# Performance work log

Measured on AMD Instinct MI355X. Metric: run time of the kernel, lower is better.

The kernel has to match this reference:

```python
import jax, jax.numpy as jnp
import numpy as np

B, N, C, H = 4, 1024, 768, 12
D = C // H
SCALE = D ** -0.5


def setup_inputs() -> dict:
    key = jax.random.key(0)
    k1, k2, k3, k4 = jax.random.split(key, 4)
    x1 = jax.random.normal(k1, (B, N, C), dtype=jnp.float32)
    x2 = jax.random.normal(k2, (B, N, C), dtype=jnp.float32)
    # shared (dual-stream) Linear2 weights, torch nn.Linear layout: [out, in]
    W_qkv = jax.random.normal(k3, (3 * C, C), dtype=jnp.float32) * (C ** -0.5)
    b_qkv = jnp.zeros((3 * C,), dtype=jnp.float32)
    W_proj = jax.random.normal(k4, (C, C), dtype=jnp.float32) * (C ** -0.5)
    b_proj = jnp.zeros((C,), dtype=jnp.float32)
    return {"x1": x1, "x2": x2, "W_qkv": W_qkv, "b_qkv": b_qkv,
            "W_proj": W_proj, "b_proj": b_proj}


def _split_qkv(x, W_qkv, b_qkv):
    qkv = (x @ W_qkv.T + b_qkv).reshape(B, N, 3, H, D)
    qkv = jnp.transpose(qkv, (2, 0, 3, 1, 4))  # [3,B,H,N,D]
    return qkv[0], qkv[1], qkv[2]


def reference(x1, x2, W_qkv, b_qkv, W_proj, b_proj):
    q1, k1, v1 = _split_qkv(x1, W_qkv, b_qkv)
    q2, k2, v2 = _split_qkv(x2, W_qkv, b_qkv)
    # two score maps, combined before a single shared softmax
    s1 = jnp.einsum("bhqd,bhkd->bhqk", q1 * SCALE, k1)
    s2 = jnp.einsum("bhqd,bhkd->bhqk", q2 * SCALE, k2)
    attn = jax.nn.softmax(s1 + s2, axis=-1)  # [B,H,N,N]
    # same attention matrix applied to both value streams
    o1 = jnp.einsum("bhqk,bhkd->bhqd", attn, v1)
    o2 = jnpum = jnp.einsum("bhqk,bhkd->bhqd", attn, v2) if False else jnp.einsum("bhqk,bhkd->bhqd", attn, v2)
    o1 = jnp.transpose(o1, (0, 2, 1, 3)).reshape(B, N, C)
    o2 = jnp.transpose(o2, (0, 2, 1, 3)).reshape(B, N, C)
    y1 = o1 @ W_proj.T + b_proj
    y2 = o2 @ W_proj.T + b_proj
    return y1, y2
```

## Files before the change

### kernel.cpp

```cpp
#include <hip/hip_runtime.h>
#include <hip/hip_bf16.h>


typedef __bf16 bf16x8 __attribute__((ext_vector_type(8)));
typedef __bf16 bf16x4 __attribute__((ext_vector_type(4)));
typedef float  f32x4  __attribute__((ext_vector_type(4)));

__device__ __forceinline__ bf16x8 cvt8(const float* p) {
    f32x4 f0 = *(const f32x4*)p;
    f32x4 f1 = *(const f32x4*)(p + 4);
    bf16x8 r;
    r[0] = (__bf16)f0[0]; r[1] = (__bf16)f0[1]; r[2] = (__bf16)f0[2]; r[3] = (__bf16)f0[3];
    r[4] = (__bf16)f1[0]; r[5] = (__bf16)f1[1]; r[6] = (__bf16)f1[2]; r[7] = (__bf16)f1[3];
    return r;
}

__device__ __forceinline__ void async16(const __bf16* g, __bf16* l) {
    __builtin_amdgcn_global_load_lds(
        (const __attribute__((address_space(1))) void*)g,
        (__attribute__((address_space(3))) void*)l, 16, 0, 0);
}

__global__ __launch_bounds__(256)
void cvt3_k(const float* __restrict__ x1, const float* __restrict__ x2,
            const float* __restrict__ wq, __bf16* __restrict__ xc,
            __bf16* __restrict__ wqc)
{
    int bid = blockIdx.x;
    const float* src; __bf16* dst; int i;
    if (bid < 1536)      { src = x1; dst = xc;             i = (bid * 256 + threadIdx.x) * 8; }
    else if (bid < 3072) { src = x2; dst = xc + 3145728;   i = ((bid - 1536) * 256 + threadIdx.x) * 8; }
    else                 { src = wq; dst = wqc;            i = ((bid - 3072) * 256 + threadIdx.x) * 8; }
    *(bf16x8*)(dst + i) = cvt8(src + i);
}

__global__ __launch_bounds__(256)
void cvt_k(const float* __restrict__ src, __bf16* __restrict__ dst, int n) {
    int i = (blockIdx.x * 256 + threadIdx.x) * 8;
    if (i < n) *(bf16x8*)(dst + i) = cvt8(src + i);
}

__global__ __launch_bounds__(256)
void gemm_qkv_s(const __bf16* __restrict__ Xc, const __bf16* __restrict__ Wq,
                const float* __restrict__ bias,
                __bf16* __restrict__ qo, __bf16* __restrict__ ko,
                __bf16* __restrict__ vo)
{
    constexpr int K = 768;
    __shared__ __bf16 As[128 * 32];
    __shared__ __bf16 Bs[128 * 32];

    const int t = threadIdx.x, w = t >> 6, lane = t & 63;
    const int l15 = lane & 15, quad = lane >> 4;
    const int wm = w >> 1, wn = w & 1;

    const int bid  = blockIdx.x;
    const int xcd  = bid & 7;
    const int i6   = bid >> 3;
    const int pair = i6 / 18;
    const int gx   = i6 - pair * 18;
    const int p    = xcd * 8 + pair;
    const int gy   = p & 31;
    const int st   = p >> 5;

    const int lrow = lane >> 2, lcol = (lane & 3) * 8;

    const __bf16* Ab = Xc + (size_t)st * 3145728 + (size_t)(gy * 128) * K;
    const __bf16* Bb = Wq + (size_t)(gx * 128) * K;

    f32x4 acc[4][4];
#pragma unroll
    for (int mi = 0; mi < 4; mi++)
#pragma unroll
        for (int ni = 0; ni < 4; ni++) acc[mi][ni] = f32x4{0.f, 0.f, 0.f, 0.f};

    for (int k0 = 0; k0 < K; k0 += 32) {
#pragma unroll
        for (int i = 0; i < 2; i++) {
            int r = w * 32 + i * 16 + lrow;
            async16(Ab + (size_t)r * K + k0 + lcol, &As[r * 32 + lcol]);
            async16(Bb + (size_t)r * K + k0 + lcol, &Bs[r * 32 + lcol]);
        }
        __syncthreads();
        bf16x8 af[4], bfr[4];
#pragma unroll
        for (int mi = 0; mi < 4; mi++)
            af[mi] = *(const bf16x8*)&As[(wm * 64 + mi * 16 + l15) * 32 + quad * 8];
#pragma unroll
        for (int ni = 0; ni < 4; ni++)
            bfr[ni] = *(const bf16x8*)&Bs[(wn * 64 + ni * 16 + l15) * 32 + quad * 8];
#pragma unroll
        for (int mi = 0; mi < 4; mi++)
#pragma unroll
            for (int ni = 0; ni < 4; ni++)
                acc[mi][ni] = __builtin_amdgcn_mfma_f32_16x16x32_bf16(af[mi], bfr[ni], acc[mi][ni], 0, 0, 0);
        __syncthreads();
    }

    const int which = (gx * 128) / 768;

    if (which == 2) {
#pragma unroll
        for (int ni = 0; ni < 4; ni++) {
            int j = gx * 128 + wn * 64 + ni * 16 + l15;
            int c = j - 1536;
            int h = c >> 6, d = c & 63;
            float bj = bias[j];
#pragma unroll
            for (int mi = 0; mi < 4; mi++) {
                int row0 = gy * 128 + wm * 64 + mi * 16 + quad * 4;
                int b = row0 >> 10, tok0 = row0 & 1023;
                bf16x4 pv;
#pragma unroll
                for (int r = 0; r < 4; r++) pv[r] = (__bf16)(acc[mi][ni][r] + bj);
                *(bf16x4*)&vo[((size_t)((st * 4 + b) * 12 + h) * 64 + d) * 1024 + tok0] = pv;
            }
        }
    } else {
#pragma unroll
        for (int ni = 0; ni < 4; ni++) {
            int j     = gx * 128 + wn * 64 + ni * 16 + l15;
            int c     = j - which * 768;
            int h = c >> 6, d = c & 63;
            float bj  = bias[j];
#pragma unroll
            for (int mi = 0; mi < 4; mi++) {
#pragma unroll
                for (int r = 0; r < 4; r++) {
                    int row = gy * 128 + wm * 64 + mi * 16 + quad * 4 + r;
                    int b = row >> 10, tok = row & 1023;
                    float val = acc[mi][ni][r] + bj;
                    if (which == 0)
                        qo[((size_t)((st * 4 + b) * 12 + h) * 1024 + tok) * 64 + d] = (__bf16)(val * 0.125f);
                    else
                        ko[((size_t)((st * 4 + b) * 12 + h) * 1024 + tok) * 64 + d] = (__bf16)val;
                }
            }
        }
    }
}

__global__ __launch_bounds__(256)
void gemm_proj(const __bf16* __restrict__ A, const __bf16* __restrict__ Wp,
               const float* __restrict__ bias, float* __restrict__ out)
{
    constexpr int K = 768;
    __shared__ __bf16 As[128 * 32];
    __shared__ __bf16 Bs[128 * 32];

    const int t = threadIdx.x, w = t >> 6, lane = t & 63;
    const int l15 = lane & 15, quad = lane >> 4;
    const int wm = w >> 1, wn = w & 1;
    const int gx = blockIdx.x, gy = blockIdx.y;
    const int lrow = lane >> 2, lcol = (lane & 3) * 8;

    const __bf16* Ab = A  + (size_t)(gy * 128) * K;
    const __bf16* Bb = Wp + (size_t)(gx * 128) * K;

    f32x4 acc[4][4];
#pragma unroll
    for (int mi = 0; mi < 4; mi++)
#pragma unroll
        for (int ni = 0; ni < 4; ni++) acc[mi][ni] = f32x4{0.f, 0.f, 0.f, 0.f};

    for (int k0 = 0; k0 < K; k0 += 32) {
#pragma unroll
        for (int i = 0; i < 2; i++) {
            int r = w * 32 + i * 16 + lrow;
            async16(Ab + (size_t)r * K + k0 + lcol, &As[r * 32 + lcol]);
            async16(Bb + (size_t)r * K + k0 + lcol, &Bs[r * 32 + lcol]);
        }
        __syncthreads();
        bf16x8 af[4], bfr[4];
#pragma unroll
        for (int mi = 0; mi < 4; mi++)
            af[mi] = *(const bf16x8*)&As[(wm * 64 + mi * 16 + l15) * 32 + quad * 8];
#pragma unroll
        for (int ni = 0; ni < 4; ni++)
            bfr[ni] = *(const bf16x8*)&Bs[(wn * 64 + ni * 16 + l15) * 32 + quad * 8];
#pragma unroll
        for (int mi = 0; mi < 4; mi++)
#pragma unroll
            for (int ni = 0; ni < 4; ni++)
                acc[mi][ni] = __builtin_amdgcn_mfma_f32_16x16x32_bf16(af[mi], bfr[ni], acc[mi][ni], 0, 0, 0);
        __syncthreads();
    }

#pragma unroll
    for (int ni = 0; ni < 4; ni++) {
        int col  = gx * 128 + wn * 64 + ni * 16 + l15;
        float bj = bias[col];
#pragma unroll
        for (int mi = 0; mi < 4; mi++)
#pragma unroll
            for (int r = 0; r < 4; r++) {
                int row = gy * 128 + wm * 64 + mi * 16 + quad * 4 + r;
                out[(size_t)row * 768 + col] = acc[mi][ni][r] + bj;
            }
    }
}

__global__ __launch_bounds__(128, 2)
void attn_k(const __bf16* __restrict__ qws, const __bf16* __restrict__ kws,
            const __bf16* __restrict__ vws, __bf16* __restrict__ ows)
{
    __shared__ __bf16 Ks[2][2][2][2][512];
    __shared__ __bf16 Vs[2][2][4][512];
    __shared__ __bf16 Ps[2][2][16 * 72];

    const int g  = blockIdx.x;
    const int qt = g / 48;
    const int bh = g % 48;
    const int b = bh / 12, h = bh % 12;
    const int t = threadIdx.x, w = t >> 6, lane = t & 63;
    const int l15 = lane & 15, quad = lane >> 4;

    const size_t head_off = (size_t)bh * 65536;
    const size_t ss       = (size_t)48 * 65536;

    bf16x8 qf[2][2][2];
#pragma unroll
    for (int set = 0; set < 2; set++)
#pragma unroll
        for (int s = 0; s < 2; s++)
#pragma unroll
            for (int kk = 0; kk < 2; kk++)
                qf[set][s][kk] = *(const bf16x8*)(qws + s * ss + head_off
                    + (size_t)(qt * 64 + w * 32 + set * 16 + l15) * 64 + kk * 32 + quad * 8);

    float lsum[2] = {0.f, 0.f};
    f32x4 accO[2][2][4];
#pragma unroll
    for (int set = 0; set < 2; set++)
#pragma unroll
        for (int s = 0; s < 2; s++)
#pragma unroll
            for (int mi = 0; mi < 4; mi++) accO[set][s][mi] = f32x4{0.f, 0.f, 0.f, 0.f};

    const __bf16* kbase = kws + head_off;
    const __bf16* vbase = vws + head_off;

#define STAGE_TILE(BUF, KEYB)                                                   \
    do {                                                                        \
        if (w == 0) {                                                           \
            _Pragma("unroll")                                                   \
            for (int i = 0; i < 8; i++) {                                       \
                const int s = i >> 2, kk = (i >> 1) & 1, mi = i & 1;            \
                async16(kbase + s * ss + (size_t)((KEYB) + mi * 16 + l15) * 64  \
                            + kk * 32 + quad * 8,                               \
                        &Ks[BUF][s][kk][mi][lane * 8]);                         \
            }                                                                   \
        } else {                                                                \
            _Pragma("unroll")                                                   \
            for (int i = 0; i < 8; i++) {                                       \
                const int s = i >> 2, mi = i & 3;                               \
                async16(vbase + s * ss + (size_t)(mi * 16 + l15) * 1024         \
                            + (KEYB) + quad * 8,                                \
                        &Vs[BUF][s][mi][lane * 8]);                             \
            }                                                                   \
        }                                                                       \
    } while (0)

    STAGE_TILE(0, 0);
    __syncthreads();

#pragma unroll 2
    for (int kt = 0; kt < 32; kt++) {
        const int cb = kt & 1, nb = cb ^ 1;

        if (kt < 31) STAGE_TILE(nb, (kt + 1) * 32);

        f32x4 accS[2][2];
#pragma unroll
        for (int set = 0; set < 2; set++)
#pragma unroll
            for (int mi = 0; mi < 2; mi++) accS[set][mi] = f32x4{0.f, 0.f, 0.f, 0.f};
        __builtin_amdgcn_s_setprio(1);
#pragma unroll
        for (int s = 0; s < 2; s++)
#pragma unroll
            for (int kk = 0; kk < 2; kk++) {
                bf16x8 kf0 = *(const bf16x8*)&Ks[cb][s][kk][0][lane * 8];
                bf16x8 kf1 = *(const bf16x8*)&Ks[cb][s][kk][1][lane * 8];
#pragma unroll
                for (int set = 0; set < 2; set++) {
                    accS[set][0] = __builtin_amdgcn_mfma_f32_16x16x32_bf16(kf0, qf[set][s][kk], accS[set][0], 0, 0, 0);
                    accS[set][1] = __builtin_amdgcn_mfma_f32_16x16x32_bf16(kf1, qf[set][s][kk], accS[set][1], 0, 0, 0);
                }
            }
        __builtin_amdgcn_s_setprio(0);

#pragma unroll
        for (int set = 0; set < 2; set++) {
            float rs = 0.f;
#pragma unroll
            for (int mi = 0; mi < 2; mi++) {
                bf16x4 pk;
#pragma unroll
                for (int r = 0; r < 4; r++) {
                    float pv = __expf(accS[set][mi][r]);
                    pk[r] = (__bf16)pv;
                    rs += pv;
                }
                *(bf16x4*)&Ps[w][set][l15 * 72 + mi * 16 + quad * 4] = pk;
            }
            lsum[set] += rs;
        }

        bf16x8 pa0 = *(const bf16x8*)&Ps[w][0][l15 * 72 + quad * 8];
        bf16x8 pa1 = *(const bf16x8*)&Ps[w][1][l15 * 72 + quad * 8];
        __builtin_amdgcn_s_setprio(1);
#pragma unroll
        for (int s = 0; s < 2; s++)
#pragma unroll
            for (int mi = 0; mi < 4; mi++) {
                bf16x8 vf = *(const bf16x8*)&Vs[cb][s][mi][lane * 8];
                accO[0][s][mi] = __builtin_amdgcn_mfma_f32_16x16x32_bf16(vf, pa0, accO[0][s][mi], 0, 0, 0);
                accO[1][s][mi] = __builtin_amdgcn_mfma_f32_16x16x32_bf16(vf, pa1, accO[1][s][mi], 0, 0, 0);
            }
        __builtin_amdgcn_s_setprio(0);

        __syncthreads();
    }
#undef STAGE_TILE

#pragma unroll
    for (int set = 0; set < 2; set++) {
        float l = lsum[set];
        l += __shfl_xor(l, 16);
        l += __shfl_xor(l, 32);
        float il = 1.f / l;

        const int tok = qt * 64 + w * 32 + set * 16 + l15;
#pragma unroll
        for (int s = 0; s < 2; s++)
#pragma unroll
            for (int mi = 0; mi < 4; mi++) {
                bf16x4 ov;
#pragma unroll
                for (int r = 0; r < 4; r++) ov[r] = (__bf16)(accO[set][s][mi][r] * il);
                *(bf16x4*)&ows[((size_t)((s * 4 + b) * 1024 + tok)) * 768
                               + h * 64 + mi * 16 + quad * 4] = ov;
            }
    }
}

extern "C" void kernel_launch(void* const* d_in, const int* in_sizes, int n_in,
                              void* d_out, int out_size, void* d_ws, size_t ws_size,
                              hipStream_t stream)
{
    const float* x1    = (const float*)d_in[0];
    const float* x2    = (const float*)d_in[1];
    const float* Wqkv  = (const float*)d_in[2];
    const float* bqkv  = (const float*)d_in[3];
    const float* Wproj = (const float*)d_in[4];
    const float* bproj = (const float*)d_in[5];
    float* out = (float*)d_out;

    const size_t qkv_elems = (size_t)2 * 4 * 12 * 1024 * 64;
    __bf16* q_ws = (__bf16*)d_ws;
    __bf16* k_ws = q_ws + qkv_elems;
    __bf16* v_ws = k_ws + qkv_elems;
    __bf16* pool = v_ws + qkv_elems;
    __bf16* Wqc  = pool + 3145728;
    __bf16* o_ws = pool;
    __bf16* Wpc  = q_ws;
    __bf16* Xc   = (__bf16*)d_out;

    cvt3_k<<<3936, 256, 0, stream>>>(x1, x2, Wqkv, Xc, Wqc);
    gemm_qkv_s<<<1152, 256, 0, stream>>>(Xc, Wqc, bqkv, q_ws, k_ws, v_ws);
    attn_k<<<768, 128, 0, stream>>>(q_ws, k_ws, v_ws, o_ws);
    cvt_k<<<288, 256, 0, stream>>>(Wproj, Wpc, 589824);
    gemm_proj<<<dim3(6, 64), 256, 0, stream>>>(o_ws, Wpc, bproj, out);
}
```

Baseline: 219.1 us.

## Triple-buffer LDS tiles in QKV and projection GEMMs with one barrier per step

Both GEMM kernels now use three LDS buffers. The next K-tile is loaded asynchronously while the current one feeds the MFMAs, with a vmcnt wait and a single barrier per iteration in place of two __syncthreads. The goal is to hide global-load latency behind compute and remove the trailing barrier. In exchange LDS use triples to 48KB per block, which may lower occupancy. Correctness now depends on the hand-written waitcnt counts and on three buffers being enough to avoid overwriting a tile that slower waves are still reading.

Result: faster. 214.0 us (-2.4%).

```diff
diff --git a/kernel.cpp b/kernel.cpp
--- a/kernel.cpp
+++ b/kernel.cpp
@@ -47,8 +47,8 @@
                 __bf16* __restrict__ vo)
 {
     constexpr int K = 768;
-    __shared__ __bf16 As[128 * 32];
-    __shared__ __bf16 Bs[128 * 32];
+    __shared__ __bf16 As[3][128 * 32];
+    __shared__ __bf16 Bs[3][128 * 32];
 
     const int t = threadIdx.x, w = t >> 6, lane = t & 63;
     const int l15 = lane & 15, quad = lane >> 4;
@@ -74,27 +74,44 @@
 #pragma unroll
         for (int ni = 0; ni < 4; ni++) acc[mi][ni] = f32x4{0.f, 0.f, 0.f, 0.f};
 
-    for (int k0 = 0; k0 < K; k0 += 32) {
-#pragma unroll
-        for (int i = 0; i < 2; i++) {
-            int r = w * 32 + i * 16 + lrow;
-            async16(Ab + (size_t)r * K + k0 + lcol, &As[r * 32 + lcol]);
-            async16(Bb + (size_t)r * K + k0 + lcol, &Bs[r * 32 + lcol]);
+#pragma unroll
+    for (int i = 0; i < 2; i++) {
+        int r = w * 32 + i * 16 + lrow;
+        async16(Ab + (size_t)r * K + lcol, &As[0][r * 32 + lcol]);
+        async16(Bb + (size_t)r * K + lcol, &Bs[0][r * 32 + lcol]);
+    }
+
+#pragma unroll 3
+    for (int kt = 0; kt < 24; kt++) {
+        const int cb = kt % 3;
+        if (kt < 23) {
+            const int nb = (kt + 1) % 3;
+            const int k0 = (kt + 1) * 32;
+#pragma unroll
+            for (int i = 0; i < 2; i++) {
+                int r = w * 32 + i * 16 + lrow;
+                async16(Ab + (size_t)r * K + k0 + lcol, &As[nb][r * 32 + lcol]);
+                async16(Bb + (size_t)r * K + k0 + lcol, &Bs[nb][r * 32 + lcol]);
+            }
+            asm volatile("s_waitcnt vmcnt(4)" ::: "memory");
+        } else {
+            asm volatile("s_waitcnt vmcnt(0)" ::: "memory");
         }
-        __syncthreads();
+        __builtin_amdgcn_s_barrier();
+        __builtin_amdgcn_sched_barrier(0);
+
         bf16x8 af[4], bfr[4];
 #pragma unroll
         for (int mi = 0; mi < 4; mi++)
-            af[mi] = *(const bf16x8*)&As[(wm * 64 + mi * 16 + l15) * 32 + quad * 8];
+            af[mi] = *(const bf16x8*)&As[cb][(wm * 64 + mi * 16 + l15) * 32 + quad * 8];
 #pragma unroll
         for (int ni = 0; ni < 4; ni++)
-            bfr[ni] = *(const bf16x8*)&Bs[(wn * 64 + ni * 16 + l15) * 32 + quad * 8];
+            bfr[ni] = *(const bf16x8*)&Bs[cb][(wn * 64 + ni * 16 + l15) * 32 + quad * 8];
 #pragma unroll
         for (int mi = 0; mi < 4; mi++)
 #pragma unroll
             for (int ni = 0; ni < 4; ni++)
                 acc[mi][ni] = __builtin_amdgcn_mfma_f32_16x16x32_bf16(af[mi], bfr[ni], acc[mi][ni], 0, 0, 0);
-        __syncthreads();
     }
 
     const int which = (gx * 128) / 768;
@@ -145,8 +162,8 @@
                const float* __restrict__ bias, float* __restrict__ out)
 {
     constexpr int K = 768;
-    __shared__ __bf16 As[128 * 32];
-    __shared__ __bf16 Bs[128 * 32];
+    __shared__ __bf16 As[3][128 * 32];
+    __shared__ __bf16 Bs[3][128 * 32];
 
     const int t = threadIdx.x, w = t >> 6, lane = t & 63;
     const int l15 = lane & 15, quad = lane >> 4;
@@ -163,27 +180,44 @@
 #pragma unroll
         for (int ni = 0; ni < 4; ni++) acc[mi][ni] = f32x4{0.f, 0.f, 0.f, 0.f};
 
-    for (int k0 = 0; k0 < K; k0 += 32) {
-#pragma unroll
-        for (int i = 0; i < 2; i++) {
-            int r = w * 32 + i * 16 + lrow;
-            async16(Ab + (size_t)r * K + k0 + lcol, &As[r * 32 + lcol]);
-            async16(Bb + (size_t)r * K + k0 + lcol, &Bs[r * 32 + lcol]);
+#pragma unroll
+    for (int i = 0; i < 2; i++) {
+        int r = w * 32 + i * 16 + lrow;
+        async16(Ab + (size_t)r * K + lcol, &As[0][r * 32 + lcol]);
+        async16(Bb + (size_t)r * K + lcol, &Bs[0][r * 32 + lcol]);
+    }
+
+#pragma unroll 3
+    for (int kt = 0; kt < 24; kt++) {
+        const int cb = kt % 3;
+        if (kt < 23) {
+            const int nb = (kt + 1) % 3;
+            const int k0 = (kt + 1) * 32;
+#pragma unroll
+            for (int i = 0; i < 2; i++) {
+                int r = w * 32 + i * 16 + lrow;
+                async16(Ab + (size_t)r * K + k0 + lcol, &As[nb][r * 32 + lcol]);
+                async16(Bb + (size_t)r * K + k0 + lcol, &Bs[nb][r * 32 + lcol]);
+            }
+            asm volatile("s_waitcnt vmcnt(4)" ::: "memory");
+        } else {
+            asm volatile("s_waitcnt vmcnt(0)" ::: "memory");
         }
-        __syncthreads();
+        __builtin_amdgcn_s_barrier();
+        __builtin_amdgcn_sched_barrier(0);
+
         bf16x8 af[4], bfr[4];
 #pragma unroll
         for (int mi = 0; mi < 4; mi++)
-            af[mi] = *(const bf16x8*)&As[(wm * 64 + mi * 16 + l15) * 32 + quad * 8];
+            af[mi] = *(const bf16x8*)&As[cb][(wm * 64 + mi * 16 + l15) * 32 + quad * 8];
 #pragma unroll
         for (int ni = 0; ni < 4; ni++)
-            bfr[ni] = *(const bf16x8*)&Bs[(wn * 64 + ni * 16 + l15) * 32 + quad * 8];
+            bfr[ni] = *(const bf16x8*)&Bs[cb][(wn * 64 + ni * 16 + l15) * 32 + quad * 8];
 #pragma unroll
         for (int mi = 0; mi < 4; mi++)
 #pragma unroll
             for (int ni = 0; ni < 4; ni++)
                 acc[mi][ni] = __builtin_amdgcn_mfma_f32_16x16x32_bf16(af[mi], bfr[ni], acc[mi][ni], 0, 0, 0);
-        __syncthreads();
     }
 
 #pragma unroll
```
